# Kernel tuning notes

Measured on AMD Instinct MI355X. Metric: run time of the kernel, lower is better.

## Reference

```python
import jax, jax.numpy as jnp
import numpy as np

N = 50000      # nodes
R = 3          # relations
E = 250000     # edges per relation
P = 100000     # candidate node pairs
F_IN = 128     # n_features
H = 256        # n_hidden
SLOPE = 0.2    # DGL GATConv default negative_slope


def setup_inputs() -> dict:
    key = jax.random.key(0)
    ks = jax.random.split(key, 14)
    s_in = 1.0 / np.sqrt(F_IN)
    s_h = 1.0 / np.sqrt(H)
    return {
        "x": jax.random.normal(ks[0], (N, F_IN), jnp.float32),
        "edges": jax.random.randint(ks[1], (R, 2, E), 0, N, jnp.int32),
        "n_pairs": jax.random.randint(ks[2], (P, 2), 0, N, jnp.int32),
        # layer 1: per-relation GATConv(F_IN -> H, 1 head)
        "W1": jax.random.normal(ks[3], (R, F_IN, H), jnp.float32) * s_in,
        "al1": jax.random.normal(ks[4], (R, H), jnp.float32) * s_h,
        "ar1": jax.random.normal(ks[5], (R, H), jnp.float32) * s_h,
        "b1": jnp.zeros((R, H), jnp.float32),
        # layer 2: per-relation GATConv(H -> F_IN, 1 head)
        "W2": jax.random.normal(ks[6], (R, H, F_IN), jnp.float32) * s_h,
        "al2": jax.random.normal(ks[7], (R, F_IN), jnp.float32) * s_in,
        "ar2": jax.random.normal(ks[8], (R, F_IN), jnp.float32) * s_in,
        "b2": jnp.zeros((R, F_IN), jnp.float32),
        # link-prediction head: Linear(2*F_IN -> 1)
        "Wlin": jax.random.normal(ks[9], (2 * F_IN, 1), jnp.float32) * (1.0 / np.sqrt(2 * F_IN)),
        "blin": jnp.zeros((1,), jnp.float32),
    }


def _gat_conv(feat_in, src, dst, W, al, ar, b):
    """Single-head DGL GATConv: projection, per-edge LeakyReLU score,
    segment-softmax over each destination's in-edges, scatter-sum messages."""
    feat = feat_in @ W                      # [N, d_out]
    el = feat @ al                          # [N]
    er = feat @ ar                          # [N]
    e = jax.nn.leaky_relu(el[src] + er[dst], SLOPE)   # [E]
    m = jax.ops.segment_max(e, dst, num_segments=N)  # per-dst max (stable softmax)
    a = jnp.exp(e - m[dst])                 # unnormalized attn
    denom = jax.ops.segment_sum(a, dst, num_segments=N)
    msg = feat[src] * a[:, None]            # [E, d_out]
    out = jax.ops.segment_sum(msg, dst, num_segments=N)
    out = out / jnp.maximum(denom, 1e-9)[:, None]
    return out + b


def reference(x, edges, n_pairs, W1, al1, ar1, b1, W2, al2, ar2, b2, Wlin, blin):
    src, dst = edges[:, 0], edges[:, 1]     # each [R, E]
    # layer 1: per-relation GAT, HeteroGraphConv mean-aggregate, then ReLU
    h1 = jax.vmap(lambda s, d, W, al, ar, b: _gat_conv(x, s, d, W, al, ar, b))(
        src, dst, W1, al1, ar1, b1)          # [R, N, H]
    h = jax.nn.relu(jnp.mean(h1, axis=0))    # [N, H]
    # layer 2: per-relation GAT on shared h, mean-aggregate
    h2 = jax.vmap(lambda s, d, W, al, ar, b: _gat_conv(h, s, d, W, al, ar, b))(
        src, dst, W2, al2, ar2, b2)          # [R, N, F_IN]
    hn = jnp.mean(h2, axis=0)                # [N, F_IN]
    # link prediction: gather endpoint features for all relation edges + n_pairs
    src_all = jnp.concatenate([src.reshape(-1), n_pairs[:, 0]])  # [R*E + P]
    dst_all = jnp.concatenate([dst.reshape(-1), n_pairs[:, 1]])
    pair_feat = jnp.concatenate([hn[src_all], hn[dst_all]], axis=1)  # [R*E+P, 2*F_IN]
    logits = jax.nn.relu(pair_feat) @ Wlin + blin
    return jax.nn.sigmoid(logits)
```

## Files before the change

kernel.cpp:

```cpp
#include <hip/hip_runtime.h>
#include <cstddef>

#define NN 50000
#define NREL 3
#define NE 250000
#define NP 100000
#define FIN 128
#define HD 256
#define SLOPE 0.2f

typedef short bf16x8 __attribute__((ext_vector_type(8)));
typedef short bf16x4 __attribute__((ext_vector_type(4)));
typedef short bf16x2 __attribute__((ext_vector_type(2)));
typedef float f32x4 __attribute__((ext_vector_type(4)));

__device__ __forceinline__ short f2bf(float f) {
  unsigned u = __float_as_uint(f);
  unsigned r = (u + 0x7FFFu + ((u >> 16) & 1u)) >> 16;
  return (short)r;
}
__device__ __forceinline__ float bf2f(short s) {
  return __uint_as_float(((unsigned)(unsigned short)s) << 16);
}

__device__ __forceinline__ void gload16(const short* g, short* l) {
  __builtin_amdgcn_global_load_lds(
      (const __attribute__((address_space(1))) unsigned int*)g,
      (__attribute__((address_space(3))) unsigned int*)l, 16, 0, 0);
}

__global__ __launch_bounds__(256) void prep_all(
    const float* __restrict__ x,  const float* __restrict__ W1,
    const float* __restrict__ W2, const float* __restrict__ al1,
    const float* __restrict__ ar1, const float* __restrict__ b1,
    const float* __restrict__ b2,
    short* __restrict__ xb, short* __restrict__ W1d, short* __restrict__ W2t,
    float* __restrict__ wvec1, float* __restrict__ beff1, float* __restrict__ beff2)
{
  const int blk = blockIdx.x;
  const int t = threadIdx.x;
  if (blk < 6250) {
    int i = (blk * 256 + t) * 4;
    float4 v = *(const float4*)&x[i];
    short4 o = {f2bf(v.x), f2bf(v.y), f2bf(v.z), f2bf(v.w)};
    *(short4*)&xb[i] = o;
  } else if (blk < 7018) {
    int o = (blk - 6250) * 256 + t;
    if (o < HD * 2 * NREL * FIN) {
      int n = o / (2 * NREL * FIN);
      int kpos = o - n * (2 * NREL * FIN);
      int ke = kpos ^ ((n & 7) << 3);
      int k2 = (ke < NREL * FIN) ? ke : ke - NREL * FIN;
      int r = k2 / FIN, kk = k2 - r * FIN;
      W1d[o] = f2bf(W1[((size_t)r * FIN + kk) * HD + n]);
    }
  } else if (blk < 7402) {
    int o = (blk - 7018) * 256 + t;
    if (o < NREL * FIN * HD) {
      int r = o / (FIN * HD);
      int rem = o - r * (FIN * HD);
      int n = rem / HD, kpos = rem - n * HD;
      int ke = kpos ^ ((n & 7) << 3);
      W2t[o] = f2bf(W2[((size_t)r * HD + ke) * FIN + n]);
    }
  } else if (blk < 7594) {
    int wid = (blk - 7402) * 4 + (t >> 6);
    int lane = t & 63;
    if (wid < 6 * FIN) {
      int j = wid / FIN, k = wid - j * FIN;
      int side = j / 3, r = j - side * 3;
      const float* v  = (side ? ar1 : al1) + r * HD;
      const float* Wr = W1 + ((size_t)r * FIN + k) * HD;
      float s = 0.f;
      for (int n = lane; n < HD; n += 64) s += Wr[n] * v[n];
#pragma unroll
      for (int off = 32; off > 0; off >>= 1) s += __shfl_down(s, off);
      if (lane == 0) wvec1[wid] = s;
    }
  } else {
    int t2 = (blk - 7594) * 256 + t;
    if (t2 < HD) beff1[t2] = (b1[t2] + b1[HD + t2] + b1[2 * HD + t2]) * (1.f / 3.f);
    else if (t2 < HD + FIN) {
      int k = t2 - HD;
      beff2[k] = (b2[k] + b2[FIN + k] + b2[2 * FIN + k]) * (1.f / 3.f);
    }
  }
}

__global__ __launch_bounds__(256) void rowdot6(
    const short* __restrict__ feat, const float* __restrict__ wvec,
    float* __restrict__ el, float* __restrict__ er)
{
  const int lane = threadIdx.x & 63;
  const int node = blockIdx.x * 4 + (threadIdx.x >> 6);
  if (node >= NN) return;
  bf16x2 f16 = *(const bf16x2*)&feat[(size_t)node * FIN + lane * 2];
  float f0 = bf2f(f16[0]), f1 = bf2f(f16[1]);
  float d[6];
#pragma unroll
  for (int j = 0; j < 6; ++j)
    d[j] = f0 * wvec[j * FIN + lane * 2] + f1 * wvec[j * FIN + lane * 2 + 1];
#pragma unroll
  for (int off = 32; off > 0; off >>= 1)
#pragma unroll
    for (int j = 0; j < 6; ++j) d[j] += __shfl_xor(d[j], off);
  if (lane == 0) {
    el[0 * NN + node] = d[0]; el[1 * NN + node] = d[1]; el[2 * NN + node] = d[2];
    er[0 * NN + node] = d[3]; er[1 * NN + node] = d[4]; er[2 * NN + node] = d[5];
  }
}

__global__ __launch_bounds__(256) void count_deg(
    const int* __restrict__ edges, int* __restrict__ deg)
{
  int tid = blockIdx.x * blockDim.x + threadIdx.x;
  if (tid >= NREL * NE) return;
  int r = tid / NE;
  int e = tid - r * NE;
  int d = edges[(size_t)r * 2 * NE + NE + e];
  atomicAdd(&deg[r * NN + d], 1);
}

__global__ __launch_bounds__(256) void deg_partial(
    const int* __restrict__ deg, int* __restrict__ psum)
{
  const int b = blockIdx.x;
  const int t = threadIdx.x;
  int4 v = {0, 0, 0, 0};
  if (t < 250) v = *(const int4*)&deg[b * 1000 + t * 4];
  int s = v.x + v.y + v.z + v.w;
#pragma unroll
  for (int off = 32; off > 0; off >>= 1) s += __shfl_down(s, off);
  __shared__ int ws[4];
  if ((t & 63) == 0) ws[t >> 6] = s;
  __syncthreads();
  if (t == 0) psum[b] = ws[0] + ws[1] + ws[2] + ws[3];
}

__global__ __launch_bounds__(256) void scan_psum(
    const int* __restrict__ psum, int* __restrict__ pexcl)
{
  __shared__ int lds[256];
  const int t = threadIdx.x;
  int v = (t < 150) ? psum[t] : 0;
  lds[t] = v;
  __syncthreads();
  for (int off = 1; off < 256; off <<= 1) {
    int add = (t >= off) ? lds[t - off] : 0;
    __syncthreads();
    lds[t] += add;
    __syncthreads();
  }
  if (t < 150) pexcl[t] = lds[t] - v;
}

__global__ __launch_bounds__(256) void deg_rowptr(
    const int* __restrict__ deg, const int* __restrict__ pexcl,
    int* __restrict__ row_ptr, int* __restrict__ cursor)
{
  const int b = blockIdx.x;
  const int t = threadIdx.x;
  int4 v = {0, 0, 0, 0};
  if (t < 250) v = *(const int4*)&deg[b * 1000 + t * 4];
  int s = v.x + v.y + v.z + v.w;
  __shared__ int lds[256];
  lds[t] = s;
  __syncthreads();
  for (int off = 1; off < 256; off <<= 1) {
    int add = (t >= off) ? lds[t - off] : 0;
    __syncthreads();
    lds[t] += add;
    __syncthreads();
  }
  int run = lds[t] - s + pexcl[b];
  if (t < 250) {
    int i = b * 1000 + t * 4;
    row_ptr[i] = run;     cursor[i] = run;     run += v.x;
    row_ptr[i + 1] = run; cursor[i + 1] = run; run += v.y;
    row_ptr[i + 2] = run; cursor[i + 2] = run; run += v.z;
    row_ptr[i + 3] = run; cursor[i + 3] = run;
  }
  if (b == 0 && t == 0) row_ptr[NREL * NN] = NREL * NE;
}

__global__ __launch_bounds__(256) void fill_csr(
    const int* __restrict__ edges, int* __restrict__ cursor,
    int* __restrict__ csr_src)
{
  int tid = blockIdx.x * blockDim.x + threadIdx.x;
  if (tid >= NREL * NE) return;
  int r = tid / NE;
  int e = tid - r * NE;
  const int* base = edges + (size_t)r * 2 * NE;
  int s = base[e];
  int d = base[NE + e];
  int pos = atomicAdd(&cursor[r * NN + d], 1);
  csr_src[pos] = s;
}

__global__ __launch_bounds__(256) void gat_gather_hl(
    const int* __restrict__ row_ptr, const int* __restrict__ csr_src,
    const float* __restrict__ el, const float* __restrict__ er,
    const short* __restrict__ xb,
    short* __restrict__ A1)
{
  const int lane  = threadIdx.x & 63;
  const int cl    = lane & 15;
  const int gbase = lane & 48;
  const int node  = blockIdx.x * 16 + (threadIdx.x >> 6) * 4 + (lane >> 4);
  if (node >= NN) return;
  const int sw = (node & 7) << 3;
  const size_t rowbase = (size_t)node * (2 * NREL * FIN);

#pragma unroll
  for (int r = 0; r < NREL; ++r) {
    const int beg = row_ptr[r * NN + node];
    const int end = row_ptr[r * NN + node + 1];
    const float eri = er[r * NN + node];
    const float* elr = el + r * NN;

    float dsum = 0.f;
    float f[8];
#pragma unroll
    for (int k = 0; k < 8; ++k) f[k] = 0.f;

    for (int chunk = beg; chunk < end; chunk += 16) {
      int e = chunk + cl;
      int sidx = 0; float a = 0.f;
      if (e < end) {
        sidx = csr_src[e];
        float tv = elr[sidx] + eri;
        tv = tv > 0.f ? tv : SLOPE * tv;
        a = __expf(tv);
      }
      dsum += a;
      const int cnt = (end - chunk < 16) ? end - chunk : 16;
      for (int i = 0; i < cnt; ++i) {
        float aj = __shfl(a, gbase + i);
        int   sj = __shfl(sidx, gbase + i);
        bf16x8 v = *(const bf16x8*)&xb[(size_t)sj * FIN + cl * 8];
#pragma unroll
        for (int k = 0; k < 8; ++k) f[k] = fmaf(bf2f(v[k]), aj, f[k]);
      }
    }
#pragma unroll
    for (int off = 8; off > 0; off >>= 1) dsum += __shfl_xor(dsum, off);
    const float inv = 1.f / (3.f * fmaxf(dsum, 1e-9f));

    bf16x8 hi, lo;
#pragma unroll
    for (int k = 0; k < 8; ++k) {
      float av = f[k] * inv;
      short hh = f2bf(av);
      hi[k] = hh;
      lo[k] = f2bf(av - bf2f(hh));
    }
    int u = (r * FIN + cl * 8) ^ sw;
    *(bf16x8*)&A1[rowbase + u] = hi;
    *(bf16x8*)&A1[rowbase + NREL * FIN + u] = lo;
  }
}

__global__ __launch_bounds__(256) void gemm_hl(
    const short* __restrict__ A, const short* __restrict__ Bt,
    const float* __restrict__ beff, short* __restrict__ hb, int M)
{
  constexpr int K = 2 * NREL * FIN;
  constexpr int BK = 64;
  __shared__ __align__(16) short AsB[(64 + 128) * BK];
  short* As = AsB;
  short* Bs = AsB + 64 * BK;
  const int tid  = threadIdx.x;
  const int lane = tid & 63;
  const int wave = tid >> 6;
  const int m0  = blockIdx.x * 64;
  const int n00 = blockIdx.y * 128;
  const int c    = lane & 15;
  const int rgrp = lane >> 4;
  const int wbase = tid & ~63;

  f32x4 acc[4][2] = {};
  for (int k0 = 0; k0 < K; k0 += BK) {
    __syncthreads();
#pragma unroll
    for (int q = 0; q < 2; ++q) {
      int idx = q * 256 + tid;
      int row = idx >> 3, ch = idx & 7;
      int gr = m0 + row; gr = gr < M ? gr : M - 1;
      gload16(&A[(size_t)gr * K + k0 + ch * 8], As + (q * 256 + wbase) * 8);
    }
#pragma unroll
    for (int q = 0; q < 4; ++q) {
      int jdx = q * 256 + tid;
      int col = jdx >> 3, ch = jdx & 7;
      gload16(&Bt[(size_t)(n00 + col) * K + k0 + ch * 8], Bs + (q * 256 + wbase) * 8);
    }
    __syncthreads();
#pragma unroll
    for (int ks = 0; ks < 2; ++ks) {
      const int ko = (ks * 32 + rgrp * 8) ^ ((c & 7) << 3);
      bf16x8 a[4], b[2];
#pragma unroll
      for (int i = 0; i < 4; ++i)
        a[i] = *(const bf16x8*)&As[(i * 16 + c) * BK + ko];
#pragma unroll
      for (int j = 0; j < 2; ++j)
        b[j] = *(const bf16x8*)&Bs[(wave * 32 + j * 16 + c) * BK + ko];
#pragma unroll
      for (int i = 0; i < 4; ++i)
#pragma unroll
        for (int j = 0; j < 2; ++j)
          acc[i][j] = __builtin_amdgcn_mfma_f32_16x16x32_bf16(a[i], b[j], acc[i][j], 0, 0, 0);
    }
  }
#pragma unroll
  for (int i = 0; i < 4; ++i)
#pragma unroll
    for (int v = 0; v < 4; ++v) {
      int row = m0 + i * 16 + rgrp * 4 + v;
      if (row < M) {
        int srow = (row & 7) << 3;
#pragma unroll
        for (int j = 0; j < 2; ++j) {
          int col = n00 + wave * 32 + j * 16 + c;
          hb[(size_t)row * HD + (col ^ srow)] =
              f2bf(fmaxf(acc[i][j][v] + beff[col], 0.f));
        }
      }
    }
}

__global__ __launch_bounds__(256) void gemm_fused2(
    const short* __restrict__ A, const short* __restrict__ Wt,
    const float* __restrict__ al, const float* __restrict__ ar,
    short* __restrict__ featb, float* __restrict__ el, float* __restrict__ er,
    int M)
{
  constexpr int K = HD;
  constexpr int BK = 64;
  constexpr int N_ = FIN;
  __shared__ __align__(16) short AsB[(64 + 128) * BK];
  __shared__ float2 part[4][64];
  short* As = AsB;
  short* Bs = AsB + 64 * BK;
  const int r = blockIdx.y;
  const short* Bt  = Wt + (size_t)r * N_ * K;
  const float* alr = al + r * N_;
  const float* arr = ar + r * N_;
  short* fb  = featb + (size_t)r * M * N_;
  float* elr = el + r * NN;
  float* err = er + r * NN;

  const int tid  = threadIdx.x;
  const int lane = tid & 63;
  const int wave = tid >> 6;
  const int m0 = blockIdx.x * 64;
  const int c    = lane & 15;
  const int rgrp = lane >> 4;
  const int wbase = tid & ~63;

  f32x4 acc[4][2] = {};
  for (int k0 = 0; k0 < K; k0 += BK) {
    __syncthreads();
#pragma unroll
    for (int q = 0; q < 2; ++q) {
      int idx = q * 256 + tid;
      int row = idx >> 3, ch = idx & 7;
      int gr = m0 + row; gr = gr < M ? gr : M - 1;
      gload16(&A[(size_t)gr * K + k0 + ch * 8], As + (q * 256 + wbase) * 8);
    }
#pragma unroll
    for (int q = 0; q < 4; ++q) {
      int jdx = q * 256 + tid;
      int col = jdx >> 3, ch = jdx & 7;
      gload16(&Bt[(size_t)col * K + k0 + ch * 8], Bs + (q * 256 + wbase) * 8);
    }
    __syncthreads();
#pragma unroll
    for (int ks = 0; ks < 2; ++ks) {
      const int ko = (ks * 32 + rgrp * 8) ^ ((c & 7) << 3);
      bf16x8 a[4], b[2];
#pragma unroll
      for (int i = 0; i < 4; ++i)
        a[i] = *(const bf16x8*)&As[(i * 16 + c) * BK + ko];
#pragma unroll
      for (int j = 0; j < 2; ++j)
        b[j] = *(const bf16x8*)&Bs[(wave * 32 + j * 16 + c) * BK + ko];
#pragma unroll
      for (int i = 0; i < 4; ++i)
#pragma unroll
        for (int j = 0; j < 2; ++j)
          acc[i][j] = __builtin_amdgcn_mfma_f32_16x16x32_bf16(a[i], b[j], acc[i][j], 0, 0, 0);
    }
  }

  float pe[4][4], pr[4][4];
#pragma unroll
  for (int i = 0; i < 4; ++i)
#pragma unroll
    for (int v = 0; v < 4; ++v) {
      float se = 0.f, sr = 0.f;
#pragma unroll
      for (int j = 0; j < 2; ++j) {
        float av = acc[i][j][v];
        int col = wave * 32 + j * 16 + c;
        se = fmaf(av, alr[col], se);
        sr = fmaf(av, arr[col], sr);
      }
      pe[i][v] = se; pr[i][v] = sr;
    }
#pragma unroll
  for (int i = 0; i < 4; ++i)
#pragma unroll
    for (int v = 0; v < 4; ++v) {
      int row = m0 + i * 16 + rgrp * 4 + v;
      if (row < M) {
#pragma unroll
        for (int j = 0; j < 2; ++j)
          fb[(size_t)row * N_ + wave * 32 + j * 16 + c] = f2bf(acc[i][j][v]);
      }
#pragma unroll
      for (int off = 1; off < 16; off <<= 1) {
        pe[i][v] += __shfl_xor(pe[i][v], off);
        pr[i][v] += __shfl_xor(pr[i][v], off);
      }
    }
  if (c == 0) {
#pragma unroll
    for (int i = 0; i < 4; ++i)
#pragma unroll
      for (int v = 0; v < 4; ++v)
        part[wave][i * 16 + rgrp * 4 + v] = make_float2(pe[i][v], pr[i][v]);
  }
  __syncthreads();
  if (tid < 64) {
    float se = 0.f, sr = 0.f;
#pragma unroll
    for (int w = 0; w < 4; ++w) { se += part[w][tid].x; sr += part[w][tid].y; }
    int row = m0 + tid;
    if (row < M) { elr[row] = se; err[row] = sr; }
  }
}

__global__ __launch_bounds__(256) void gat_agg_dots(
    const int* __restrict__ row_ptr, const int* __restrict__ csr_src,
    const float* __restrict__ el, const float* __restrict__ er,
    const short* __restrict__ featb,
    const float* __restrict__ beff,
    const float* __restrict__ Wlin,
    float* __restrict__ dotl, float* __restrict__ dotr)
{
  const int lane  = threadIdx.x & 63;
  const int cl    = lane & 15;
  const int gbase = lane & 48;
  const int node  = blockIdx.x * 16 + (threadIdx.x >> 6) * 4 + (lane >> 4);
  if (node >= NN) return;

  float t[8];
#pragma unroll
  for (int k = 0; k < 8; ++k) t[k] = 0.f;

#pragma unroll
  for (int r = 0; r < NREL; ++r) {
    const int beg = row_ptr[r * NN + node];
    const int end = row_ptr[r * NN + node + 1];
    const float eri = er[r * NN + node];
    const float* elr = el + r * NN;
    const short* fb  = featb + (size_t)r * NN * FIN;

    float dsum = 0.f;
    float f[8];
#pragma unroll
    for (int k = 0; k < 8; ++k) f[k] = 0.f;

    for (int chunk = beg; chunk < end; chunk += 16) {
      int e = chunk + cl;
      int sidx = 0; float a = 0.f;
      if (e < end) {
        sidx = csr_src[e];
        float tv = elr[sidx] + eri;
        tv = tv > 0.f ? tv : SLOPE * tv;
        a = __expf(tv);
      }
      dsum += a;
      const int cnt = (end - chunk < 16) ? end - chunk : 16;
      for (int i = 0; i < cnt; ++i) {
        float aj = __shfl(a, gbase + i);
        int   sj = __shfl(sidx, gbase + i);
        bf16x8 v = *(const bf16x8*)&fb[(size_t)sj * FIN + cl * 8];
#pragma unroll
        for (int k = 0; k < 8; ++k) f[k] = fmaf(bf2f(v[k]), aj, f[k]);
      }
    }
#pragma unroll
    for (int off = 8; off > 0; off >>= 1) dsum += __shfl_xor(dsum, off);
    const float inv = 1.f / (3.f * fmaxf(dsum, 1e-9f));
#pragma unroll
    for (int k = 0; k < 8; ++k) t[k] = fmaf(f[k], inv, t[k]);
  }

  const int c = cl * 8;
  float dl = 0.f, dr = 0.f;
#pragma unroll
  for (int k = 0; k < 8; ++k) {
    float g = fmaxf(t[k] + beff[c + k], 0.f);
    dl = fmaf(g, Wlin[c + k], dl);
    dr = fmaf(g, Wlin[FIN + c + k], dr);
  }
#pragma unroll
  for (int off = 8; off > 0; off >>= 1) {
    dl += __shfl_xor(dl, off);
    dr += __shfl_xor(dr, off);
  }
  if (cl == 0) { dotl[node] = dl; dotr[node] = dr; }
}

__global__ __launch_bounds__(256) void pair_out(
    const int* __restrict__ edges, const int* __restrict__ n_pairs,
    const float* __restrict__ dotl, const float* __restrict__ dotr,
    const float* __restrict__ blin, float* __restrict__ out)
{
  const int TOT = NREL * NE + NP;
  int p = blockIdx.x * blockDim.x + threadIdx.x;
  if (p >= TOT) return;
  int s, d;
  if (p < NREL * NE) {
    int r = p / NE;
    int e = p - r * NE;
    const int* base = edges + (size_t)r * 2 * NE;
    s = base[e];
    d = base[NE + e];
  } else {
    int q = p - NREL * NE;
    s = n_pairs[2 * q];
    d = n_pairs[2 * q + 1];
  }
  float logit = dotl[s] + dotr[d] + blin[0];
  out[p] = 1.f / (1.f + expf(-logit));
}

extern "C" void kernel_launch(void* const* d_in, const int* in_sizes, int n_in,
                              void* d_out, int out_size, void* d_ws, size_t ws_size,
                              hipStream_t stream) {
  const float* x      = (const float*)d_in[0];
  const int*   edges  = (const int*)d_in[1];
  const int*   npairs = (const int*)d_in[2];
  const float* W1     = (const float*)d_in[3];
  const float* al1    = (const float*)d_in[4];
  const float* ar1    = (const float*)d_in[5];
  const float* b1     = (const float*)d_in[6];
  const float* W2     = (const float*)d_in[7];
  const float* al2    = (const float*)d_in[8];
  const float* ar2    = (const float*)d_in[9];
  const float* b2     = (const float*)d_in[10];
  const float* Wlin   = (const float*)d_in[11];
  const float* blin   = (const float*)d_in[12];
  float* out = (float*)d_out;

  char* w = (char*)d_ws;
  size_t off = 0;
  auto alloc = [&](size_t bytes) {
    char* p = w + off;
    off = (off + bytes + 255) & ~(size_t)255;
    return p;
  };
  short* xb      = (short*)alloc((size_t)NN * FIN * 2);
  short* hb      = (short*)alloc((size_t)NN * HD * 2);
  short* A1      = (short*)alloc((size_t)NN * 2 * NREL * FIN * 2);
  short* featb2  = A1;
  short* W1d     = (short*)alloc((size_t)HD * 2 * NREL * FIN * 2);
  short* W2t     = (short*)alloc((size_t)NREL * FIN * HD * 2);
  float* wvec1   = (float*)alloc(6 * FIN * 4);
  float* beff1   = (float*)alloc(HD * 4);
  float* beff2   = (float*)alloc(FIN * 4);
  float* el      = (float*)alloc((size_t)NREL * NN * 4);
  float* er      = (float*)alloc((size_t)NREL * NN * 4);
  float* dotl    = (float*)alloc((size_t)NN * 4);
  float* dotr    = (float*)alloc((size_t)NN * 4);
  int*   deg     = (int*)  alloc((size_t)NREL * NN * 4);
  int*   cursor  = (int*)  alloc((size_t)NREL * NN * 4);
  int*   row_ptr = (int*)  alloc((size_t)(NREL * NN + 16) * 4);
  int*   psum    = (int*)  alloc(1024);
  int*   pexcl   = (int*)  alloc(1024);
  int*   csr_src = (int*)  alloc((size_t)NREL * NE * 4);

  const int B = 256;

  prep_all<<<7596, B, 0, stream>>>(x, W1, W2, al1, ar1, b1, b2,
                                   xb, W1d, W2t, wvec1, beff1, beff2);

  hipMemsetAsync(deg, 0, (size_t)NREL * NN * 4, stream);
  count_deg<<<(NREL * NE + B - 1) / B, B, 0, stream>>>(edges, deg);
  deg_partial<<<150, B, 0, stream>>>(deg, psum);
  scan_psum<<<1, B, 0, stream>>>(psum, pexcl);
  deg_rowptr<<<150, B, 0, stream>>>(deg, pexcl, row_ptr, cursor);
  fill_csr<<<(NREL * NE + B - 1) / B, B, 0, stream>>>(edges, cursor, csr_src);

  const int AGG_G  = (NN + 3) / 4;
  const int AGG16  = (NN + 15) / 16;
  const int GEMM_GX = (NN + 63) / 64;

  rowdot6<<<AGG_G, B, 0, stream>>>(xb, wvec1, el, er);
  gat_gather_hl<<<AGG16, B, 0, stream>>>(row_ptr, csr_src, el, er, xb, A1);
  {
    dim3 g(GEMM_GX, 2);
    gemm_hl<<<g, B, 0, stream>>>(A1, W1d, beff1, hb, NN);
  }

  {
    dim3 g(GEMM_GX, NREL);
    gemm_fused2<<<g, B, 0, stream>>>(hb, W2t, al2, ar2, featb2, el, er, NN);
  }
  gat_agg_dots<<<AGG16, B, 0, stream>>>(row_ptr, csr_src, el, er, featb2,
                                        beff2, Wlin, dotl, dotr);

  const int TOT = NREL * NE + NP;
  pair_out<<<(TOT + B - 1) / B, B, 0, stream>>>(edges, npairs, dotl, dotr, blin, out);
}
```

Measured before the change: 275.6 us.

## Replace bf16 hi/lo split with single fp16 operand in layer-1 GEMM

The aggregated layer-1 features were stored as a bf16 hi/lo pair, which doubled the GEMM K dimension to compensate for precision. They are now stored as one fp16 value, the weights are converted to fp16, and the GEMM uses the fp16 MFMA, halving both A1 traffic and MFMA work. The GEMM also now covers all 256 output columns per block instead of using two y-blocks, so A tiles are loaded once. fp16 trades range for mantissa, so large aggregated values could overflow or lose accuracy compared with the hi/lo bf16 scheme.

```diff
diff --git a/kernel.cpp b/kernel.cpp
--- a/kernel.cpp
+++ b/kernel.cpp
@@ -8,11 +8,12 @@
 #define FIN 128
 #define HD 256
 #define SLOPE 0.2f
+#define K1 (NREL * FIN)
 
 typedef short bf16x8 __attribute__((ext_vector_type(8)));
-typedef short bf16x4 __attribute__((ext_vector_type(4)));
 typedef short bf16x2 __attribute__((ext_vector_type(2)));
 typedef float f32x4 __attribute__((ext_vector_type(4)));
+typedef _Float16 half8 __attribute__((ext_vector_type(8)));
 
 __device__ __forceinline__ short f2bf(float f) {
   unsigned u = __float_as_uint(f);
@@ -44,27 +45,22 @@
     float4 v = *(const float4*)&x[i];
     short4 o = {f2bf(v.x), f2bf(v.y), f2bf(v.z), f2bf(v.w)};
     *(short4*)&xb[i] = o;
+  } else if (blk < 6634) {
+    int o = (blk - 6250) * 256 + t;
+    int n = o / K1;
+    int kpos = o - n * K1;
+    int ke = kpos ^ ((n & 7) << 3);
+    int r = ke / FIN, kk = ke - r * FIN;
+    ((_Float16*)W1d)[o] = (_Float16)W1[((size_t)r * FIN + kk) * HD + n];
   } else if (blk < 7018) {
-    int o = (blk - 6250) * 256 + t;
-    if (o < HD * 2 * NREL * FIN) {
-      int n = o / (2 * NREL * FIN);
-      int kpos = o - n * (2 * NREL * FIN);
-      int ke = kpos ^ ((n & 7) << 3);
-      int k2 = (ke < NREL * FIN) ? ke : ke - NREL * FIN;
-      int r = k2 / FIN, kk = k2 - r * FIN;
-      W1d[o] = f2bf(W1[((size_t)r * FIN + kk) * HD + n]);
-    }
-  } else if (blk < 7402) {
-    int o = (blk - 7018) * 256 + t;
-    if (o < NREL * FIN * HD) {
-      int r = o / (FIN * HD);
-      int rem = o - r * (FIN * HD);
-      int n = rem / HD, kpos = rem - n * HD;
-      int ke = kpos ^ ((n & 7) << 3);
-      W2t[o] = f2bf(W2[((size_t)r * HD + ke) * FIN + n]);
-    }
-  } else if (blk < 7594) {
-    int wid = (blk - 7402) * 4 + (t >> 6);
+    int o = (blk - 6634) * 256 + t;
+    int r = o / (FIN * HD);
+    int rem = o - r * (FIN * HD);
+    int n = rem / HD, kpos = rem - n * HD;
+    int ke = kpos ^ ((n & 7) << 3);
+    W2t[o] = f2bf(W2[((size_t)r * HD + ke) * FIN + n]);
+  } else if (blk < 7210) {
+    int wid = (blk - 7018) * 4 + (t >> 6);
     int lane = t & 63;
     if (wid < 6 * FIN) {
       int j = wid / FIN, k = wid - j * FIN;
@@ -78,7 +74,7 @@
       if (lane == 0) wvec1[wid] = s;
     }
   } else {
-    int t2 = (blk - 7594) * 256 + t;
+    int t2 = (blk - 7210) * 256 + t;
     if (t2 < HD) beff1[t2] = (b1[t2] + b1[HD + t2] + b1[2 * HD + t2]) * (1.f / 3.f);
     else if (t2 < HD + FIN) {
       int k = t2 - HD;
@@ -210,7 +206,7 @@
   const int node  = blockIdx.x * 16 + (threadIdx.x >> 6) * 4 + (lane >> 4);
   if (node >= NN) return;
   const int sw = (node & 7) << 3;
-  const size_t rowbase = (size_t)node * (2 * NREL * FIN);
+  const size_t rowbase = (size_t)node * K1;
 
 #pragma unroll
   for (int r = 0; r < NREL; ++r) {
@@ -247,17 +243,11 @@
     for (int off = 8; off > 0; off >>= 1) dsum += __shfl_xor(dsum, off);
     const float inv = 1.f / (3.f * fmaxf(dsum, 1e-9f));
 
-    bf16x8 hi, lo;
-#pragma unroll
-    for (int k = 0; k < 8; ++k) {
-      float av = f[k] * inv;
-      short hh = f2bf(av);
-      hi[k] = hh;
-      lo[k] = f2bf(av - bf2f(hh));
-    }
+    half8 hv;
+#pragma unroll
+    for (int k = 0; k < 8; ++k) hv[k] = (_Float16)(f[k] * inv);
     int u = (r * FIN + cl * 8) ^ sw;
-    *(bf16x8*)&A1[rowbase + u] = hi;
-    *(bf16x8*)&A1[rowbase + NREL * FIN + u] = lo;
+    *(half8*)&A1[rowbase + u] = hv;
   }
 }
 
@@ -265,52 +255,51 @@
     const short* __restrict__ A, const short* __restrict__ Bt,
     const float* __restrict__ beff, short* __restrict__ hb, int M)
 {
-  constexpr int K = 2 * NREL * FIN;
   constexpr int BK = 64;
-  __shared__ __align__(16) short AsB[(64 + 128) * BK];
+  __shared__ __align__(16) short AsB[(64 + 256) * BK];
   short* As = AsB;
   short* Bs = AsB + 64 * BK;
   const int tid  = threadIdx.x;
   const int lane = tid & 63;
   const int wave = tid >> 6;
-  const int m0  = blockIdx.x * 64;
-  const int n00 = blockIdx.y * 128;
+  const int m0 = blockIdx.x * 64;
+  const int n0 = wave * 64;
   const int c    = lane & 15;
   const int rgrp = lane >> 4;
   const int wbase = tid & ~63;
 
-  f32x4 acc[4][2] = {};
-  for (int k0 = 0; k0 < K; k0 += BK) {
+  f32x4 acc[4][4] = {};
+  for (int k0 = 0; k0 < K1; k0 += BK) {
     __syncthreads();
 #pragma unroll
     for (int q = 0; q < 2; ++q) {
       int idx = q * 256 + tid;
       int row = idx >> 3, ch = idx & 7;
       int gr = m0 + row; gr = gr < M ? gr : M - 1;
-      gload16(&A[(size_t)gr * K + k0 + ch * 8], As + (q * 256 + wbase) * 8);
-    }
-#pragma unroll
-    for (int q = 0; q < 4; ++q) {
+      gload16(&A[(size_t)gr * K1 + k0 + ch * 8], As + (q * 256 + wbase) * 8);
+    }
+#pragma unroll
+    for (int q = 0; q < 8; ++q) {
       int jdx = q * 256 + tid;
       int col = jdx >> 3, ch = jdx & 7;
-      gload16(&Bt[(size_t)(n00 + col) * K + k0 + ch * 8], Bs + (q * 256 + wbase) * 8);
+      gload16(&Bt[(size_t)col * K1 + k0 + ch * 8], Bs + (q * 256 + wbase) * 8);
     }
     __syncthreads();
 #pragma unroll
     for (int ks = 0; ks < 2; ++ks) {
       const int ko = (ks * 32 + rgrp * 8) ^ ((c & 7) << 3);
-      bf16x8 a[4], b[2];
+      half8 a[4], b[4];
 #pragma unroll
       for (int i = 0; i < 4; ++i)
-        a[i] = *(const bf16x8*)&As[(i * 16 + c) * BK + ko];
-#pragma unroll
-      for (int j = 0; j < 2; ++j)
-        b[j] = *(const bf16x8*)&Bs[(wave * 32 + j * 16 + c) * BK + ko];
+        a[i] = *(const half8*)&As[(i * 16 + c) * BK + ko];
+#pragma unroll
+      for (int j = 0; j < 4; ++j)
+        b[j] = *(const half8*)&Bs[(n0 + j * 16 + c) * BK + ko];
 #pragma unroll
       for (int i = 0; i < 4; ++i)
 #pragma unroll
-        for (int j = 0; j < 2; ++j)
-          acc[i][j] = __builtin_amdgcn_mfma_f32_16x16x32_bf16(a[i], b[j], acc[i][j], 0, 0, 0);
+        for (int j = 0; j < 4; ++j)
+          acc[i][j] = __builtin_amdgcn_mfma_f32_16x16x32_f16(a[i], b[j], acc[i][j], 0, 0, 0);
     }
   }
 #pragma unroll
@@ -321,8 +310,8 @@
       if (row < M) {
         int srow = (row & 7) << 3;
 #pragma unroll
-        for (int j = 0; j < 2; ++j) {
-          int col = n00 + wave * 32 + j * 16 + c;
+        for (int j = 0; j < 4; ++j) {
+          int col = n0 + j * 16 + c;
           hb[(size_t)row * HD + (col ^ srow)] =
               f2bf(fmaxf(acc[i][j][v] + beff[col], 0.f));
         }
@@ -566,9 +555,9 @@
   };
   short* xb      = (short*)alloc((size_t)NN * FIN * 2);
   short* hb      = (short*)alloc((size_t)NN * HD * 2);
-  short* A1      = (short*)alloc((size_t)NN * 2 * NREL * FIN * 2);
+  short* A1      = (short*)alloc((size_t)NN * K1 * 2);
   short* featb2  = A1;
-  short* W1d     = (short*)alloc((size_t)HD * 2 * NREL * FIN * 2);
+  short* W1d     = (short*)alloc((size_t)HD * K1 * 2);
   short* W2t     = (short*)alloc((size_t)NREL * FIN * HD * 2);
   float* wvec1   = (float*)alloc(6 * FIN * 4);
   float* beff1   = (float*)alloc(HD * 4);
@@ -586,7 +575,7 @@
 
   const int B = 256;
 
-  prep_all<<<7596, B, 0, stream>>>(x, W1, W2, al1, ar1, b1, b2,
+  prep_all<<<7212, B, 0, stream>>>(x, W1, W2, al1, ar1, b1, b2,
                                    xb, W1d, W2t, wvec1, beff1, beff2);
 
   hipMemsetAsync(deg, 0, (size_t)NREL * NN * 4, stream);
@@ -602,10 +591,7 @@
 
   rowdot6<<<AGG_G, B, 0, stream>>>(xb, wvec1, el, er);
   gat_gather_hl<<<AGG16, B, 0, stream>>>(row_ptr, csr_src, el, er, xb, A1);
-  {
-    dim3 g(GEMM_GX, 2);
-    gemm_hl<<<g, B, 0, stream>>>(A1, W1d, beff1, hb, NN);
-  }
+  gemm_hl<<<GEMM_GX, B, 0, stream>>>(A1, W1d, beff1, hb, NN);
 
   {
     dim3 g(GEMM_GX, NREL);
```

Result: faster. 257.3 us (-6.6%).
